# Kernel optimization log

Hardware: AMD Instinct MI355X
Metric: run time of the kernel (lower is better)

Reference implementation:

```python
import jax, jax.numpy as jnp
import numpy as np

HEADS = 16
HEAD_DIM = 128
ROPE_BASE = 10000.0

def _rope_tables(T, D):
    # inv_freq over even indices, freqs = outer(pos, inv_freq), emb = concat([freqs, freqs])
    inv_freq = 1.0 / (ROPE_BASE ** (jnp.arange(0, D, 2, dtype=jnp.float32) / D))
    t = jnp.arange(T, dtype=jnp.float32)
    freqs = t[:, None] * inv_freq[None, :]          # (T, D/2)
    emb = jnp.concatenate([freqs, freqs], axis=-1)  # (T, D)
    return jnp.cos(emb), jnp.sin(emb)

def _rotate_half(x):
    half = x.shape[-1] // 2
    x1, x2 = x[..., :half], x[..., half:]
    return jnp.concatenate([-x2, x1], axis=-1)

def setup_inputs() -> dict:
    key = jax.random.key(0)
    k1, k2, k3 = jax.random.split(key, 3)
    B, T, dim = 2, 2048, 2048
    inner = HEADS * HEAD_DIM
    x = jax.random.normal(k1, (B, T, dim), dtype=jnp.float32)
    W_qkv = jax.random.normal(k2, (3 * inner, dim), dtype=jnp.float32) * 0.02
    W_proj = jax.random.normal(k3, (dim, inner), dtype=jnp.float32) * 0.02
    return {"x": x, "W_qkv": W_qkv, "W_proj": W_proj}

def reference(x, W_qkv, W_proj):
    B, T, dim = x.shape
    H, D = HEADS, HEAD_DIM
    # QKV projection (Linear with weight (out, in): y = x @ W^T)
    qkv = jnp.einsum('btd,ed->bte', x, W_qkv)          # (B, T, 3*H*D)
    q, k, v = jnp.split(qkv, 3, axis=-1)
    def to_heads(t):
        return t.reshape(B, T, H, D).transpose(0, 2, 1, 3)  # (B, H, T, D)
    q, k, v = to_heads(q), to_heads(k), to_heads(v)
    # RoPE, offset = 0 (uncached path)
    cos, sin = _rope_tables(T, D)                      # (T, D)
    cos = cos[None, None]
    sin = sin[None, None]
    q = q * cos + _rotate_half(q) * sin
    k = k * cos + _rotate_half(k) * sin
    # causal SDPA
    scale = 1.0 / jnp.sqrt(jnp.float32(D))
    scores = jnp.einsum('bhqd,bhkd->bhqk', q, k) * scale
    causal = jnp.tril(jnp.ones((T, T), dtype=bool))
    scores = jnp.where(causal[None, None], scores, jnp.finfo(scores.dtype).min)
    attn = jax.nn.softmax(scores, axis=-1)
    out = jnp.einsum('bhqk,bhkd->bhqd', attn, v)       # (B, H, T, D)
    out = out.transpose(0, 2, 1, 3).reshape(B, T, H * D)
    return jnp.einsum('bti,oi->bto', out, W_proj)      # (B, T, dim)
```

## Files before the change

### kernel.cpp

```cpp
#include <hip/hip_runtime.h>
#include <hip/hip_bf16.h>
#include <stdint.h>

typedef __attribute__((ext_vector_type(8))) short short8;
typedef __attribute__((ext_vector_type(4))) float f32x4;

#define HEADS 16
#define HDIM  128
#define BB    2
#define TT    2048
#define DMODEL 2048
#define INNER 2048
#define E3    6144
#define NTOK  (BB*TT)

__device__ inline void store1(__hip_bfloat16* p, float v) { *p = __float2bfloat16(v); }
__device__ inline void store1(float* p, float v)          { *p = v; }

__device__ inline short bfbits(float v) {
  __hip_bfloat16 h = __float2bfloat16(v);
  return *(short*)&h;
}

__device__ inline void gl_lds16(const __hip_bfloat16* g, __hip_bfloat16* l) {
  __builtin_amdgcn_global_load_lds(
      (const __attribute__((address_space(1))) void*)g,
      (__attribute__((address_space(3))) void*)l, 16, 0, 0);
}

__device__ inline void cvt8(const float* in, __hip_bfloat16* out, int i) {
  float4 a = *(const float4*)(in + i);
  float4 b = *(const float4*)(in + i + 4);
  short8 r;
  r[0]=bfbits(a.x); r[1]=bfbits(a.y); r[2]=bfbits(a.z); r[3]=bfbits(a.w);
  r[4]=bfbits(b.x); r[5]=bfbits(b.y); r[6]=bfbits(b.z); r[7]=bfbits(b.w);
  *(short8*)(out + i) = r;
}

#define NBX   (NTOK*DMODEL/2048)
#define NBW   (E3*DMODEL/2048)
#define NBT   (TT*64/256)
__global__ __launch_bounds__(256)
void prep(const float* __restrict__ x, const float* __restrict__ Wqkv,
          __hip_bfloat16* __restrict__ xb, __hip_bfloat16* __restrict__ Wqkvb,
          float2* __restrict__ tab)
{
  const int tid = threadIdx.x;
  int blk = blockIdx.x;
  if (blk < NBX) {
    cvt8(x, xb, (blk*256 + tid)*8);
  } else if (blk < NBX + NBW) {
    cvt8(Wqkv, Wqkvb, ((blk-NBX)*256 + tid)*8);
  } else {
    int idx = (blk - NBX - NBW)*256 + tid;
    int t  = idx >> 6;
    int d2 = idx & 63;
    float inv = powf(10000.f, -(float)d2 * (1.f/64.f));
    float ang = (float)t * inv;
    tab[idx] = make_float2(cosf(ang), sinf(ang));
  }
}

__global__ __launch_bounds__(256)
void cvt_bf16(const float* __restrict__ in, __hip_bfloat16* __restrict__ out, int n)
{
  int i = (blockIdx.x * 256 + threadIdx.x) * 8;
  if (i >= n) return;
  cvt8(in, out, i);
}

template<typename TC>
__global__ __launch_bounds__(256, 2)
void gemm_lds(const __hip_bfloat16* __restrict__ A,
              const __hip_bfloat16* __restrict__ B,
              TC* __restrict__ C,
              int M, int N, int K)
{
  __shared__ __hip_bfloat16 sA[128*32];
  __shared__ __hip_bfloat16 sB[128*32];
  const int tid  = threadIdx.x;
  const int lane = tid & 63;
  const int wv   = tid >> 6;
  const int lm   = lane & 15;
  const int quad = lane >> 4;
  const int wm   = (wv >> 1) * 64;
  const int wn   = (wv & 1) * 64;
  const int bm   = blockIdx.y * 128;
  const int bn   = blockIdx.x * 128;

  f32x4 acc[4][4];
  #pragma unroll
  for (int i=0;i<4;i++)
    #pragma unroll
    for (int j=0;j<4;j++) acc[i][j] = (f32x4){0.f,0.f,0.f,0.f};

  const int srow = wv*32 + (lane >> 2);
  const int scol = (lane & 3) * 8;
  const __hip_bfloat16* gA0 = A + (size_t)(bm + srow)*K + scol;
  const __hip_bfloat16* gA1 = gA0 + (size_t)16*K;
  const __hip_bfloat16* gB0 = B + (size_t)(bn + srow)*K + scol;
  const __hip_bfloat16* gB1 = gB0 + (size_t)16*K;
  __hip_bfloat16* lA0 = sA + wv*1024;
  __hip_bfloat16* lA1 = lA0 + 512;
  __hip_bfloat16* lB0 = sB + wv*1024;
  __hip_bfloat16* lB1 = lB0 + 512;

  for (int k0 = 0; k0 < K; k0 += 32) {
    __syncthreads();
    gl_lds16(gA0, lA0);
    gl_lds16(gA1, lA1);
    gl_lds16(gB0, lB0);
    gl_lds16(gB1, lB1);
    gA0 += 32; gA1 += 32; gB0 += 32; gB1 += 32;
    __syncthreads();
    short8 af[4], bf[4];
    #pragma unroll
    for (int t=0;t<4;t++)
      af[t] = *(const short8*)(sA + (wm + t*16 + lm)*32 + quad*8);
    #pragma unroll
    for (int t=0;t<4;t++)
      bf[t] = *(const short8*)(sB + (wn + t*16 + lm)*32 + quad*8);
    #pragma unroll
    for (int i=0;i<4;i++)
      #pragma unroll
      for (int j=0;j<4;j++)
        acc[i][j] = __builtin_amdgcn_mfma_f32_16x16x32_bf16(af[i], bf[j], acc[i][j], 0,0,0);
  }

  const int row0 = bm + wm + quad*4;
  const int col0 = bn + wn + lm;
  #pragma unroll
  for (int i=0;i<4;i++)
    #pragma unroll
    for (int j=0;j<4;j++)
      #pragma unroll
      for (int r=0;r<4;r++)
        store1(C + (size_t)(row0 + i*16 + r)*N + col0 + j*16, acc[i][j][r]);
}

__global__ __launch_bounds__(256, 2)
void gemm_qkv(const __hip_bfloat16* __restrict__ A,
              const __hip_bfloat16* __restrict__ B,
              const float2* __restrict__ tab,
              __hip_bfloat16* __restrict__ Qh,
              __hip_bfloat16* __restrict__ Kh,
              __hip_bfloat16* __restrict__ Vt)
{
  __shared__ __hip_bfloat16 smem[128*130];
  __hip_bfloat16* sA = smem;
  __hip_bfloat16* sB = smem + 128*32;
  __hip_bfloat16* sT = smem;
  const int tid  = threadIdx.x;
  const int lane = tid & 63;
  const int wv   = tid >> 6;
  const int lm   = lane & 15;
  const int quad = lane >> 4;
  const int wm   = (wv >> 1) * 64;
  const int wn   = (wv & 1) * 64;
  const int bm   = blockIdx.y * 128;
  const int bn   = blockIdx.x * 128;

  f32x4 acc[4][4];
  #pragma unroll
  for (int i=0;i<4;i++)
    #pragma unroll
    for (int j=0;j<4;j++) acc[i][j] = (f32x4){0.f,0.f,0.f,0.f};

  const int srow = wv*32 + (lane >> 2);
  const int scol = (lane & 3) * 8;
  const __hip_bfloat16* gA0 = A + (size_t)(bm + srow)*DMODEL + scol;
  const __hip_bfloat16* gA1 = gA0 + (size_t)16*DMODEL;
  const __hip_bfloat16* gB0 = B + (size_t)(bn + srow)*DMODEL + scol;
  const __hip_bfloat16* gB1 = gB0 + (size_t)16*DMODEL;
  __hip_bfloat16* lA0 = sA + wv*1024;
  __hip_bfloat16* lA1 = lA0 + 512;
  __hip_bfloat16* lB0 = sB + wv*1024;
  __hip_bfloat16* lB1 = lB0 + 512;

  for (int k0 = 0; k0 < DMODEL; k0 += 32) {
    __syncthreads();
    gl_lds16(gA0, lA0);
    gl_lds16(gA1, lA1);
    gl_lds16(gB0, lB0);
    gl_lds16(gB1, lB1);
    gA0 += 32; gA1 += 32; gB0 += 32; gB1 += 32;
    __syncthreads();
    short8 af[4], bf[4];
    #pragma unroll
    for (int t=0;t<4;t++)
      af[t] = *(const short8*)(sA + (wm + t*16 + lm)*32 + quad*8);
    #pragma unroll
    for (int t=0;t<4;t++)
      bf[t] = *(const short8*)(sB + (wn + t*16 + lm)*32 + quad*8);
    #pragma unroll
    for (int i=0;i<4;i++)
      #pragma unroll
      for (int j=0;j<4;j++)
        acc[i][j] = __builtin_amdgcn_mfma_f32_16x16x32_bf16(af[i], bf[j], acc[i][j], 0,0,0);
  }

  __syncthreads();

  const int trow = wm + quad*4;
  const int tcol = wn + lm;
  #pragma unroll
  for (int i=0;i<4;i++)
    #pragma unroll
    for (int j=0;j<4;j++)
      #pragma unroll
      for (int r=0;r<4;r++)
        sT[(trow + i*16 + r)*130 + tcol + j*16] = __float2bfloat16(acc[i][j][r]);
  __syncthreads();

  const int type = bn >> 11;
  const int h    = (bn >> 7) & 15;
  const int bgl  = bm >> 11;
  const int tl0  = bm & (TT-1);
  const size_t bh = (size_t)bgl*HEADS + h;
  const float SCQ = 0.08838834764831845f * 1.4426950408889634f;

  if (type < 2) {
    __hip_bfloat16* dst = (type == 0) ? Qh : Kh;
    const float mul = (type == 0) ? SCQ : 1.0f;
    #pragma unroll
    for (int p=0;p<4;p++) {
      const int rowl = p*32 + (tid >> 3);
      const int d2b  = (tid & 7) * 8;
      const int t    = tl0 + rowl;
      const float2* tp = tab + (size_t)t*64 + d2b;
      short8 o1, o2;
      #pragma unroll
      for (int k=0;k<8;k++) {
        float2 cs = tp[k];
        float v1 = __bfloat162float(sT[rowl*130 + d2b + k]);
        float v2 = __bfloat162float(sT[rowl*130 + d2b + k + 64]);
        o1[k] = bfbits((v1*cs.x - v2*cs.y) * mul);
        o2[k] = bfbits((v2*cs.x + v1*cs.y) * mul);
      }
      __hip_bfloat16* o = dst + (bh*TT + t)*HDIM + d2b;
      *(short8*)o        = o1;
      *(short8*)(o + 64) = o2;
    }
  } else {
    #pragma unroll
    for (int it2=0; it2<8; ++it2) {
      const int sidx = it2*256 + tid;
      const int d  = sidx >> 4;
      const int tc = (sidx & 15) * 8;
      short8 o;
      #pragma unroll
      for (int k=0;k<8;k++) o[k] = *(const short*)&sT[(tc+k)*130 + d];
      *(short8*)(Vt + (bh*HDIM + d)*TT + tl0 + tc) = o;
    }
  }
}

__global__ __launch_bounds__(256, 3)
void flash_attn(const __hip_bfloat16* __restrict__ Qh,
                const __hip_bfloat16* __restrict__ Kh,
                const __hip_bfloat16* __restrict__ Vt,
                __hip_bfloat16* __restrict__ Out)
{
  const int tid  = threadIdx.x;
  const int lane = tid & 63;
  const int wv   = tid >> 6;
  const int lm   = lane & 15;
  const int quad = lane >> 4;
  const int jA   = blockIdx.x;
  const int bh   = blockIdx.y;
  const int b    = bh >> 4;
  const int h    = bh & 15;

  __shared__ __hip_bfloat16 sK[64*136];
  __shared__ __hip_bfloat16 sV[128*72];
  __shared__ __hip_bfloat16 sP[4][16*72];

  const float FML2 = 8.0f * 1.4426950408889634f;

  const int rk0 = tid >> 4;
  const int ck  = (tid & 15) * 8;
  const int dv0 = tid >> 3;
  const int cv  = (tid & 7) * 8;
  const __hip_bfloat16* KpBase = Kh + (size_t)bh*TT*HDIM + (size_t)rk0*HDIM + ck;
  const __hip_bfloat16* VpBase = Vt + (size_t)bh*HDIM*TT + (size_t)dv0*TT + cv;

  #pragma unroll
  for (int pass = 0; pass < 2; ++pass) {
    const int q0 = (pass == 0 ? jA : 31 - jA) * 64;

    short8 aq[4];
    {
      const __hip_bfloat16* qp = Qh + ((size_t)bh*TT + q0 + wv*16 + lm)*HDIM + quad*8;
      #pragma unroll
      for (int kd=0;kd<4;kd++) aq[kd] = *(const short8*)(qp + kd*32);
    }

    float l_p[4] = {0,0,0,0};
    f32x4 acc_o[8];
    #pragma unroll
    for (int i=0;i<8;i++) acc_o[i] = (f32x4){0.f,0.f,0.f,0.f};

    const __hip_bfloat16* Kp = KpBase;
    const __hip_bfloat16* Vp = VpBase;
    short8 pk[4], pv[4];
    #pragma unroll
    for (int it=0;it<4;++it) {
      pk[it] = *(const short8*)(Kp + (size_t)it*16*HDIM);
      pv[it] = *(const short8*)(Vp + (size_t)it*32*TT);
    }
    Kp += (size_t)64*HDIM; Vp += 64;

    for (int kv0 = 0; kv0 <= q0; kv0 += 64) {
      __syncthreads();
      #pragma unroll
      for (int it=0;it<4;++it) {
        *(short8*)(&sK[(it*16 + rk0)*136 + ck]) = pk[it];
        *(short8*)(&sV[(it*32 + dv0)*72 + cv])  = pv[it];
      }
      if (kv0 + 64 <= q0) {
        #pragma unroll
        for (int it=0;it<4;++it) {
          pk[it] = *(const short8*)(Kp + (size_t)it*16*HDIM);
          pv[it] = *(const short8*)(Vp + (size_t)it*32*TT);
        }
        Kp += (size_t)64*HDIM; Vp += 64;
      }
      __syncthreads();

      f32x4 accs[4];
      #pragma unroll
      for (int nt=0;nt<4;nt++) accs[nt] = (f32x4){0.f,0.f,0.f,0.f};
      #pragma unroll
      for (int kd=0;kd<4;kd++)
        #pragma unroll
        for (int nt=0;nt<4;nt++) {
          short8 bk = *(const short8*)(&sK[(nt*16 + lm)*136 + kd*32 + quad*8]);
          accs[nt] = __builtin_amdgcn_mfma_f32_16x16x32_bf16(aq[kd], bk, accs[nt], 0,0,0);
        }

      const int rowb = q0 + wv*16 + quad*4;
      const bool diag = (kv0 == q0);
      #pragma unroll
      for (int nt=0;nt<4;nt++)
        #pragma unroll
        for (int r=0;r<4;r++) {
          float p = exp2f(accs[nt][r] - FML2);
          if (diag && (kv0 + nt*16 + lm > rowb + r)) p = 0.f;
          l_p[r] += p;
          sP[wv][(quad*4 + r)*72 + nt*16 + lm] = __float2bfloat16(p);
        }

      #pragma unroll
      for (int kd2=0;kd2<2;kd2++) {
        short8 ap = *(const short8*)(&sP[wv][lm*72 + kd2*32 + quad*8]);
        #pragma unroll
        for (int nt2=0;nt2<8;nt2++) {
          short8 bvv = *(const short8*)(&sV[(nt2*16 + lm)*72 + kd2*32 + quad*8]);
          acc_o[nt2] = __builtin_amdgcn_mfma_f32_16x16x32_bf16(ap, bvv, acc_o[nt2], 0,0,0);
        }
      }
    }

    #pragma unroll
    for (int off=1; off<16; off<<=1)
      #pragma unroll
      for (int r=0;r<4;r++) l_p[r] += __shfl_xor(l_p[r], off);
    #pragma unroll
    for (int r=0;r<4;r++) l_p[r] = 1.f / l_p[r];

    #pragma unroll
    for (int nt2=0;nt2<8;nt2++)
      #pragma unroll
      for (int r=0;r<4;r++) {
        int t = q0 + wv*16 + quad*4 + r;
        Out[((size_t)b*TT + t)*INNER + (size_t)h*HDIM + nt2*16 + lm] =
          __float2bfloat16(acc_o[nt2][r] * l_p[r]);
      }
  }
}

extern "C" void kernel_launch(void* const* d_in, const int* in_sizes, int n_in,
                              void* d_out, int out_size, void* d_ws, size_t ws_size,
                              hipStream_t stream)
{
  (void)in_sizes; (void)n_in; (void)out_size; (void)ws_size;
  const float* x     = (const float*)d_in[0];
  const float* Wqkv  = (const float*)d_in[1];
  const float* Wproj = (const float*)d_in[2];
  float* out = (float*)d_out;

  char* ws = (char*)d_ws;
  __hip_bfloat16* xb       = (__hip_bfloat16*)ws;
  __hip_bfloat16* attn_out = xb;
  char* p1 = ws + (size_t)NTOK*DMODEL*2;
  __hip_bfloat16* Wqkvb  = (__hip_bfloat16*)p1;
  __hip_bfloat16* Wprojb = (__hip_bfloat16*)p1;
  char* p2 = p1 + (size_t)E3*DMODEL*2;
  float2* ropeTab = (float2*)p2;
  char* p3 = p2 + (size_t)DMODEL*INNER*2;
  const size_t hsz = (size_t)BB*HEADS*TT*HDIM*2;
  __hip_bfloat16* Qh = (__hip_bfloat16*)p3;
  __hip_bfloat16* Kh = (__hip_bfloat16*)(p3 + hsz);
  __hip_bfloat16* Vt = (__hip_bfloat16*)(p3 + 2*hsz);

  prep<<<dim3(NBX + NBW + NBT), dim3(256), 0, stream>>>(x, Wqkv, xb, Wqkvb, ropeTab);

  gemm_qkv<<<dim3(E3/128, NTOK/128), dim3(256), 0, stream>>>(xb, Wqkvb, ropeTab, Qh, Kh, Vt);

  cvt_bf16<<<dim3(DMODEL*INNER/2048), dim3(256), 0, stream>>>(Wproj, Wprojb, DMODEL*INNER);

  flash_attn<<<dim3(TT/128, BB*HEADS), dim3(256), 0, stream>>>(Qh, Kh, Vt, attn_out);

  gemm_lds<float>
    <<<dim3(INNER/128, NTOK/128), dim3(256), 0, stream>>>(attn_out, Wprojb, out, NTOK, INNER, DMODEL);
}
```

Baseline: 383.8 us.

## Rewrite QKV GEMM with 256x256 tiles, double-buffered swizzled LDS and fused epilogue

```diff
diff --git a/kernel.cpp b/kernel.cpp
--- a/kernel.cpp
+++ b/kernel.cpp
@@ -3,6 +3,7 @@
 #include <stdint.h>
 
 typedef __attribute__((ext_vector_type(8))) short short8;
+typedef __attribute__((ext_vector_type(4))) short short4v;
 typedef __attribute__((ext_vector_type(4))) float f32x4;
 
 #define HEADS 16
@@ -138,119 +139,164 @@
         store1(C + (size_t)(row0 + i*16 + r)*N + col0 + j*16, acc[i][j][r]);
 }
 
-__global__ __launch_bounds__(256, 2)
-void gemm_qkv(const __hip_bfloat16* __restrict__ A,
-              const __hip_bfloat16* __restrict__ B,
-              const float2* __restrict__ tab,
-              __hip_bfloat16* __restrict__ Qh,
-              __hip_bfloat16* __restrict__ Kh,
-              __hip_bfloat16* __restrict__ Vt)
-{
-  __shared__ __hip_bfloat16 smem[128*130];
-  __hip_bfloat16* sA = smem;
-  __hip_bfloat16* sB = smem + 128*32;
-  __hip_bfloat16* sT = smem;
+__global__ __launch_bounds__(512, 2)
+void gemm_qkv2(const __hip_bfloat16* __restrict__ A,
+               const __hip_bfloat16* __restrict__ B,
+               const float2* __restrict__ tab,
+               __hip_bfloat16* __restrict__ Qh,
+               __hip_bfloat16* __restrict__ Kh,
+               __hip_bfloat16* __restrict__ Vt)
+{
+  __shared__ __align__(128) __hip_bfloat16 smem[65536];
   const int tid  = threadIdx.x;
   const int lane = tid & 63;
-  const int wv   = tid >> 6;
+  const int w    = tid >> 6;
   const int lm   = lane & 15;
   const int quad = lane >> 4;
-  const int wm   = (wv >> 1) * 64;
-  const int wn   = (wv & 1) * 64;
-  const int bm   = blockIdx.y * 128;
-  const int bn   = blockIdx.x * 128;
-
-  f32x4 acc[4][4];
+  const int wm   = w >> 2;
+  const int wn   = w & 3;
+
+  const int flat  = blockIdx.x;
+  const int wgid  = (flat & 7) * 48 + (flat >> 3);
+  const int tileN = wgid >> 4;
+  const int tileM = wgid & 15;
+  const int bm    = tileM << 8;
+  const int bn    = tileN << 8;
+  const int type  = bn >> 11;
+
+  const int r0 = tid >> 3;
+  const int kc = (tid & 7) ^ (r0 & 7);
+  size_t gA[2][2], gB[2][2];
   #pragma unroll
-  for (int i=0;i<4;i++)
+  for (int h = 0; h < 2; ++h)
+    #pragma unroll
+    for (int j = 0; j < 2; ++j) {
+      gA[h][j] = ((size_t)(bm + h*128 + j*64 + r0) << 11) + kc*8;
+      int prow;
+      if (type < 2)
+        prow = h*128 + j*32 + ((r0 >> 5) << 6) + (((r0 >> 4) & 1) << 4) + (r0 & 15);
+      else
+        prow = h*128 + j*64 + r0;
+      gB[h][j] = ((size_t)(bn + prow) << 11) + kc*8;
+    }
+  const int ldsW = w * 512;
+
+#define STAGE_A(h, ktt, bb_) do { \
+    __hip_bfloat16* _l = smem + (bb_)*32768 + (h)*8192 + ldsW; \
+    gl_lds16(A + gA[h][0] + (size_t)(ktt)*64, _l); \
+    gl_lds16(A + gA[h][1] + (size_t)(ktt)*64, _l + 4096); \
+  } while (0)
+#define STAGE_B(h, ktt, bb_) do { \
+    __hip_bfloat16* _l = smem + (bb_)*32768 + 16384 + (h)*8192 + ldsW; \
+    gl_lds16(B + gB[h][0] + (size_t)(ktt)*64, _l); \
+    gl_lds16(B + gB[h][1] + (size_t)(ktt)*64, _l + 4096); \
+  } while (0)
+
+  const int xk0 = ((quad      ^ (lm & 7)) << 3);
+  const int xk1 = (((quad|4)  ^ (lm & 7)) << 3);
+  const int aRow = wm*8192 + lm*64;
+  const int bRow = 16384 + (wn>>1)*8192 + (wn&1)*4096 + lm*64;
+
+  f32x4 acc[8][4];
+  #pragma unroll
+  for (int i=0;i<8;i++)
     #pragma unroll
     for (int j=0;j<4;j++) acc[i][j] = (f32x4){0.f,0.f,0.f,0.f};
 
-  const int srow = wv*32 + (lane >> 2);
-  const int scol = (lane & 3) * 8;
-  const __hip_bfloat16* gA0 = A + (size_t)(bm + srow)*DMODEL + scol;
-  const __hip_bfloat16* gA1 = gA0 + (size_t)16*DMODEL;
-  const __hip_bfloat16* gB0 = B + (size_t)(bn + srow)*DMODEL + scol;
-  const __hip_bfloat16* gB1 = gB0 + (size_t)16*DMODEL;
-  __hip_bfloat16* lA0 = sA + wv*1024;
-  __hip_bfloat16* lA1 = lA0 + 512;
-  __hip_bfloat16* lB0 = sB + wv*1024;
-  __hip_bfloat16* lB1 = lB0 + 512;
-
-  for (int k0 = 0; k0 < DMODEL; k0 += 32) {
-    __syncthreads();
-    gl_lds16(gA0, lA0);
-    gl_lds16(gA1, lA1);
-    gl_lds16(gB0, lB0);
-    gl_lds16(gB1, lB1);
-    gA0 += 32; gA1 += 32; gB0 += 32; gB1 += 32;
-    __syncthreads();
-    short8 af[4], bf[4];
-    #pragma unroll
-    for (int t=0;t<4;t++)
-      af[t] = *(const short8*)(sA + (wm + t*16 + lm)*32 + quad*8);
-    #pragma unroll
-    for (int t=0;t<4;t++)
-      bf[t] = *(const short8*)(sB + (wn + t*16 + lm)*32 + quad*8);
-    #pragma unroll
-    for (int i=0;i<4;i++)
-      #pragma unroll
-      for (int j=0;j<4;j++)
-        acc[i][j] = __builtin_amdgcn_mfma_f32_16x16x32_bf16(af[i], bf[j], acc[i][j], 0,0,0);
+  STAGE_A(0, 0, 0); STAGE_A(1, 0, 0);
+  STAGE_B(0, 0, 0); STAGE_B(1, 0, 0);
+  STAGE_B(0, 1, 1); STAGE_B(1, 1, 1);
+  asm volatile("s_waitcnt vmcnt(4)" ::: "memory");
+  __builtin_amdgcn_s_barrier();
+
+  #pragma unroll 2
+  for (int kt = 0; kt < 32; ++kt) {
+    const int cb   = kt & 1;
+    const int nb   = cb ^ 1;
+    const int cOff = cb * 32768;
+    short8 bfrag[4][2];
+    #pragma unroll
+    for (int q = 0; q < 4; ++q) {
+      if (q == 0) {
+        #pragma unroll
+        for (int f = 0; f < 4; ++f) {
+          bfrag[f][0] = *(const short8*)(smem + cOff + bRow + f*1024 + xk0);
+          bfrag[f][1] = *(const short8*)(smem + cOff + bRow + f*1024 + xk1);
+        }
+      }
+      short8 a0s0 = *(const short8*)(smem + cOff + aRow + (q*2+0)*1024 + xk0);
+      short8 a0s1 = *(const short8*)(smem + cOff + aRow + (q*2+0)*1024 + xk1);
+      short8 a1s0 = *(const short8*)(smem + cOff + aRow + (q*2+1)*1024 + xk0);
+      short8 a1s1 = *(const short8*)(smem + cOff + aRow + (q*2+1)*1024 + xk1);
+      if (q == 0)      { if (kt + 1 < 32) { STAGE_A(0, kt+1, nb); STAGE_A(1, kt+1, nb); } }
+      else if (q == 1) { if (kt + 2 < 32) STAGE_B(0, kt+2, cb); }
+      else if (q == 2) { if (kt + 2 < 32) STAGE_B(1, kt+2, cb); }
+      __builtin_amdgcn_s_barrier();
+      __builtin_amdgcn_s_setprio(1);
+      #pragma unroll
+      for (int nf = 0; nf < 4; ++nf) {
+        acc[q*2+0][nf] = __builtin_amdgcn_mfma_f32_16x16x32_bf16(a0s0, bfrag[nf][0], acc[q*2+0][nf], 0,0,0);
+        acc[q*2+0][nf] = __builtin_amdgcn_mfma_f32_16x16x32_bf16(a0s1, bfrag[nf][1], acc[q*2+0][nf], 0,0,0);
+        acc[q*2+1][nf] = __builtin_amdgcn_mfma_f32_16x16x32_bf16(a1s0, bfrag[nf][0], acc[q*2+1][nf], 0,0,0);
+        acc[q*2+1][nf] = __builtin_amdgcn_mfma_f32_16x16x32_bf16(a1s1, bfrag[nf][1], acc[q*2+1][nf], 0,0,0);
+      }
+      __builtin_amdgcn_s_setprio(0);
+      if (q < 3) {
+        __builtin_amdgcn_s_barrier();
+      } else {
+        if (kt < 30) asm volatile("s_waitcnt vmcnt(4)" ::: "memory");
+        else         asm volatile("s_waitcnt vmcnt(0)" ::: "memory");
+        __builtin_amdgcn_s_barrier();
+      }
+    }
   }
-
-  __syncthreads();
-
-  const int trow = wm + quad*4;
-  const int tcol = wn + lm;
-  #pragma unroll
-  for (int i=0;i<4;i++)
-    #pragma unroll
-    for (int j=0;j<4;j++)
-      #pragma unroll
-      for (int r=0;r<4;r++)
-        sT[(trow + i*16 + r)*130 + tcol + j*16] = __float2bfloat16(acc[i][j][r]);
-  __syncthreads();
-
-  const int type = bn >> 11;
-  const int h    = (bn >> 7) & 15;
-  const int bgl  = bm >> 11;
-  const int tl0  = bm & (TT-1);
-  const size_t bh = (size_t)bgl*HEADS + h;
+#undef STAGE_A
+#undef STAGE_B
+
   const float SCQ = 0.08838834764831845f * 1.4426950408889634f;
-
+  const int tok0 = bm + wm*128;
   if (type < 2) {
-    __hip_bfloat16* dst = (type == 0) ? Qh : Kh;
+    __hip_bfloat16* const dst = (type == 0) ? Qh : Kh;
     const float mul = (type == 0) ? SCQ : 1.0f;
-    #pragma unroll
-    for (int p=0;p<4;p++) {
-      const int rowl = p*32 + (tid >> 3);
-      const int d2b  = (tid & 7) * 8;
-      const int t    = tl0 + rowl;
-      const float2* tp = tab + (size_t)t*64 + d2b;
-      short8 o1, o2;
-      #pragma unroll
-      for (int k=0;k<8;k++) {
-        float2 cs = tp[k];
-        float v1 = __bfloat162float(sT[rowl*130 + d2b + k]);
-        float v2 = __bfloat162float(sT[rowl*130 + d2b + k + 64]);
-        o1[k] = bfbits((v1*cs.x - v2*cs.y) * mul);
-        o2[k] = bfbits((v2*cs.x + v1*cs.y) * mul);
-      }
-      __hip_bfloat16* o = dst + (bh*TT + t)*HDIM + d2b;
-      *(short8*)o        = o1;
-      *(short8*)(o + 64) = o2;
+    const int head = ((bn & 2047) >> 7) + (wn >> 1);
+    const int d2b  = (wn & 1)*32 + lm;
+    #pragma unroll
+    for (int i = 0; i < 8; ++i) {
+      #pragma unroll
+      for (int r = 0; r < 4; ++r) {
+        const int t  = tok0 + i*16 + quad*4 + r;
+        const int b  = t >> 11;
+        const int tl = t & (TT-1);
+        const float2* tp = tab + (size_t)tl*64;
+        __hip_bfloat16* const o = dst + ((size_t)(b*HEADS + head)*TT + tl)*HDIM;
+        #pragma unroll
+        for (int j = 0; j < 2; ++j) {
+          const int d2 = d2b + j*16;
+          const float2 cs = tp[d2];
+          const float v1 = acc[i][j  ][r];
+          const float v2 = acc[i][j+2][r];
+          o[d2]      = __float2bfloat16((v1*cs.x - v2*cs.y) * mul);
+          o[d2 + 64] = __float2bfloat16((v2*cs.x + v1*cs.y) * mul);
+        }
+      }
     }
   } else {
-    #pragma unroll
-    for (int it2=0; it2<8; ++it2) {
-      const int sidx = it2*256 + tid;
-      const int d  = sidx >> 4;
-      const int tc = (sidx & 15) * 8;
-      short8 o;
-      #pragma unroll
-      for (int k=0;k<8;k++) o[k] = *(const short*)&sT[(tc+k)*130 + d];
-      *(short8*)(Vt + (bh*HDIM + d)*TT + tl0 + tc) = o;
+    const int fcb = (bn & 2047) + wn*64 + lm;
+    #pragma unroll
+    for (int i = 0; i < 8; ++i) {
+      const int t0 = tok0 + i*16 + quad*4;
+      const int b  = t0 >> 11;
+      const int tl = t0 & (TT-1);
+      #pragma unroll
+      for (int j = 0; j < 4; ++j) {
+        const int c    = fcb + j*16;
+        const int head = c >> 7;
+        const int d    = c & 127;
+        short4v o;
+        #pragma unroll
+        for (int r = 0; r < 4; ++r) o[r] = bfbits(acc[i][j][r]);
+        *(short4v*)(Vt + ((size_t)(b*HEADS + head)*HDIM + d)*TT + tl) = o;
+      }
     }
   }
 }
@@ -405,7 +451,7 @@
 
   prep<<<dim3(NBX + NBW + NBT), dim3(256), 0, stream>>>(x, Wqkv, xb, Wqkvb, ropeTab);
 
-  gemm_qkv<<<dim3(E3/128, NTOK/128), dim3(256), 0, stream>>>(xb, Wqkvb, ropeTab, Qh, Kh, Vt);
+  gemm_qkv2<<<dim3(384), dim3(512), 0, stream>>>(xb, Wqkvb, ropeTab, Qh, Kh, Vt);
 
   cvt_bf16<<<dim3(DMODEL*INNER/2048), dim3(256), 0, stream>>>(Wproj, Wprojb, DMODEL*INNER);
 
```

Result: no change. 381.2 us (-0.7%).
